# Kernel tuning notes

Measured on AMD Instinct MI355X. Metric: run time of the kernel, lower is better.

Reference implementation:

```python
import jax, jax.numpy as jnp
import numpy as np
from jax import lax

EPS = 1e-5


def _conv3x3(inp, w):
    # NCHW input, OIHW kernel, VALID padding, stride 1 (matches nn.Conv2d(k=3, s=1, p=0))
    return lax.conv_general_dilated(inp, w, (1, 1), 'VALID',
                                    dimension_numbers=('NCHW', 'OIHW', 'NCHW'))


def _bn(h, gamma, beta, mean, var):
    # inference-mode BatchNorm2d
    inv = gamma / jnp.sqrt(var + EPS)
    return h * inv[None, :, None, None] + (beta - mean * inv)[None, :, None, None]


def _xcorr_depthwise(zf, xf):
    # per-sample, per-channel sliding cross-correlation: template zf over search xf
    B, C, Hz, Wz = zf.shape
    _, _, Hx, Wx = xf.shape
    xr = xf.reshape(1, B * C, Hx, Wx)
    kr = zf.reshape(B * C, 1, Hz, Wz)
    out = lax.conv_general_dilated(xr, kr, (1, 1), 'VALID',
                                   feature_group_count=B * C,
                                   dimension_numbers=('NCHW', 'OIHW', 'NCHW'))
    return out.reshape(B, C, out.shape[2], out.shape[3])


def setup_inputs() -> dict:
    key = jax.random.key(0)
    ks = jax.random.split(key, 12)
    B, Cin, Ch = 64, 256, 256
    z = jax.random.normal(ks[0], (B, Cin, 16, 16), dtype=jnp.float32)
    x = jax.random.normal(ks[1], (B, Cin, 32, 32), dtype=jnp.float32)
    # conv weights ~ N(0, 0.01) as in _initialize_weights
    w_z = 0.01 * jax.random.normal(ks[2], (Ch, Cin, 3, 3), dtype=jnp.float32)
    w_x = 0.01 * jax.random.normal(ks[3], (Ch, Cin, 3, 3), dtype=jnp.float32)
    gamma_z = 0.5 + jax.random.uniform(ks[4], (Ch,), dtype=jnp.float32)
    beta_z = 0.1 * jax.random.normal(ks[5], (Ch,), dtype=jnp.float32)
    mean_z = 0.1 * jax.random.normal(ks[6], (Ch,), dtype=jnp.float32)
    var_z = 0.5 + jax.random.uniform(ks[7], (Ch,), dtype=jnp.float32)
    gamma_x = 0.5 + jax.random.uniform(ks[8], (Ch,), dtype=jnp.float32)
    beta_x = 0.1 * jax.random.normal(ks[9], (Ch,), dtype=jnp.float32)
    mean_x = 0.1 * jax.random.normal(ks[10], (Ch,), dtype=jnp.float32)
    var_x = 0.5 + jax.random.uniform(ks[11], (Ch,), dtype=jnp.float32)
    return {'z': z, 'x': x, 'w_z': w_z, 'w_x': w_x,
            'gamma_z': gamma_z, 'beta_z': beta_z, 'mean_z': mean_z, 'var_z': var_z,
            'gamma_x': gamma_x, 'beta_x': beta_x, 'mean_x': mean_x, 'var_x': var_x}


def reference(z, x, w_z, w_x, gamma_z, beta_z, mean_z, var_z,
              gamma_x, beta_x, mean_x, var_x):
    zf = _bn(_conv3x3(z, w_z), gamma_z, beta_z, mean_z, var_z)   # [B,C,14,14]
    xf = _bn(_conv3x3(x, w_x), gamma_x, beta_x, mean_x, var_x)   # [B,C,30,30]
    return _xcorr_depthwise(zf, xf)                               # [B,C,17,17]
```

## Files before the change

### kernel.cpp

```cpp
#include <hip/hip_runtime.h>
#include <cstdint>
#include <cstddef>

typedef _Float16 f16;
typedef _Float16 half4 __attribute__((ext_vector_type(4)));
typedef _Float16 half8 __attribute__((ext_vector_type(8)));
typedef float f32x4 __attribute__((ext_vector_type(4)));

#define BN_EPS 1e-5f

static constexpr size_t OFF_XB  = 0;
static constexpr size_t OFF_ZB  = 33554432;
static constexpr size_t OFF_WX  = 41943040;
static constexpr size_t OFF_WZ  = 43122688;
static constexpr size_t OFF_BNX = 44302336;
static constexpr size_t OFF_BNZ = 44304384;
static constexpr size_t OFF_XFH = 44306432;
static constexpr size_t OFF_ZFH = 75763712;

__global__ __launch_bounds__(256) void prep_all(
    const float* __restrict__ x, const float* __restrict__ z,
    const float* __restrict__ w_x, const float* __restrict__ w_z,
    const float* __restrict__ gx, const float* __restrict__ bx,
    const float* __restrict__ mx, const float* __restrict__ vx,
    const float* __restrict__ gz, const float* __restrict__ bz,
    const float* __restrict__ mz, const float* __restrict__ vz,
    f16* __restrict__ xb, f16* __restrict__ zb,
    f16* __restrict__ wxA, f16* __restrict__ wzA,
    float* __restrict__ bnx, float* __restrict__ bnz) {
  __shared__ float tile[64][33];
  const int bid = blockIdx.x;
  const int tid = threadIdx.x;
  if (bid < 12288) {
    const float* src; f16* dst; int lw, r;
    if (bid < 8192) { src = x; dst = xb; lw = 5; r = bid; }
    else            { src = z; dst = zb; lw = 4; r = bid - 8192; }
    const int W = 1 << lw;
    const int c0 = (r & 3) << 6;
    const int h = (r >> 2) & (W - 1);
    const int b = (r >> 2) >> lw;
    const float* sp = src + (size_t)(((b << 8) + c0) << lw << lw) + ((size_t)h << lw);
    const int n = W << 6;
    for (int i = tid; i < n; i += 256) {
      int cl = i >> lw, w = i & (W - 1);
      tile[cl][w] = sp[(size_t)cl << lw << lw | w];
    }
    __syncthreads();
    f16* dp = dst + ((size_t)((b << lw) + h) << lw << 8) + c0;
    for (int i = tid; i < n; i += 256) {
      int w = i >> 6, cl = i & 63;
      dp[(w << 8) + cl] = (f16)tile[cl][w];
    }
  } else if (bid < 16896) {
    int r = bid - 12288;
    const float* src = (r < 2304) ? w_x : w_z;
    f16* dst = (r < 2304) ? wxA : wzA;
    int rr = (r < 2304) ? r : r - 2304;
    int idx = rr * 256 + tid;
    int cin = idx & 255, cout = (idx >> 8) & 255, khw = idx >> 16;
    dst[idx] = (f16)src[(cout * 256 + cin) * 9 + khw];
  } else {
    int c = tid;
    float iv = gx[c] / sqrtf(vx[c] + BN_EPS);
    bnx[c] = iv;
    bnx[256 + c] = bx[c] - mx[c] * iv;
    float iz = gz[c] / sqrtf(vz[c] + BN_EPS);
    bnz[c] = iz;
    bnz[256 + c] = bz[c] - mz[c] * iz;
  }
}

__device__ __forceinline__ void gl_lds16(const f16* g, f16* l) {
  __builtin_amdgcn_global_load_lds((__attribute__((address_space(1))) void*)g,
                                   (__attribute__((address_space(3))) void*)l, 16, 0, 0);
}

__global__ __launch_bounds__(256, 4) void conv_gemm_u(
    const f16* __restrict__ xb, const f16* __restrict__ zb,
    const f16* __restrict__ wx, const f16* __restrict__ wz,
    const float* __restrict__ bnx, const float* __restrict__ bnz,
    f16* __restrict__ xfh, f16* __restrict__ zfh) {
  __shared__ f16 As[128 * 64];
  __shared__ f16 Bs[128 * 64];
  const int g = blockIdx.x;
  const int pairIdx = ((g >> 4) << 3) | (g & 7);
  const int mblk = (g >> 3) & 1;
  if (pairIdx >= 548) return;
  const f16* inp; const f16* wA; const float* bn; f16* out;
  int nblk, HIN, WIN, WOUT, NPIX, WPAD, OPLANE;
  if (pairIdx < 450) {
    inp = xb; wA = wx; bn = bnx; out = xfh; nblk = pairIdx;
    HIN = 32; WIN = 32; WOUT = 30; NPIX = 900; WPAD = 32; OPLANE = 960;
  } else {
    inp = zb; wA = wz; bn = bnz; out = zfh; nblk = pairIdx - 450;
    HIN = 16; WIN = 16; WOUT = 14; NPIX = 196; WPAD = 16; OPLANE = 224;
  }
  const int tid = threadIdx.x;
  const int wid = tid >> 6, lane = tid & 63;
  const int wm = (wid >> 1) << 6, wn = (wid & 1) << 6;
  const int q = lane >> 4, lm = lane & 15;
  const int sr = lane >> 3, sc = lane & 7;
  const int swz = (sc ^ sr) << 3;
  const int mbase = mblk << 7;

  int arow[4], brow[4];
#pragma unroll
  for (int l = 0; l < 4; ++l) {
    int rr = (wid << 5) + (l << 3) + sr;
    arow[l] = ((mbase + rr) << 8) + swz;
    int n = (nblk << 7) + rr;
    int b = n / NPIX, rem = n - b * NPIX;
    int oh = rem / WOUT, ow = rem - oh * WOUT;
    brow[l] = (((b * HIN + oh) * WIN + ow) << 8) + swz;
  }

  f32x4 acc[4][4] = {};
  const int cA0 = (q ^ (lm & 7)) << 3;

  for (int kt = 0; kt < 36; ++kt) {
    const int cinb = kt / 9;
    const int khw = kt - cinb * 9;
    const int cin0 = cinb << 6;
    const int kh = khw / 3, kw = khw - kh * 3;
    const int wofs = (khw << 16) + cin0;
    const int iofs = ((kh * WIN + kw) << 8) + cin0;
#pragma unroll
    for (int l = 0; l < 4; ++l) {
      const int ldso = ((wid << 5) + (l << 3)) << 6;
      gl_lds16(wA + wofs + arow[l], As + ldso);
      gl_lds16(inp + iofs + brow[l], Bs + ldso);
    }
    __syncthreads();
#pragma unroll
    for (int h = 0; h < 2; ++h) {
      const int co = cA0 ^ (h << 5);
      half8 af[4], bf[4];
#pragma unroll
      for (int f = 0; f < 4; ++f) {
        af[f] = *(const half8*)&As[((wm + (f << 4) + lm) << 6) + co];
        bf[f] = *(const half8*)&Bs[((wn + (f << 4) + lm) << 6) + co];
      }
#pragma unroll
      for (int fm = 0; fm < 4; ++fm)
#pragma unroll
        for (int fn = 0; fn < 4; ++fn)
          acc[fm][fn] =
              __builtin_amdgcn_mfma_f32_16x16x32_f16(af[fm], bf[fn], acc[fm][fn], 0, 0, 0);
    }
    __syncthreads();
  }

#pragma unroll
  for (int fn = 0; fn < 4; ++fn) {
    int n_g = (nblk << 7) + wn + (fn << 4) + lm;
    int b = n_g / NPIX, rem = n_g - b * NPIX;
    int oh = rem / WOUT, ow = rem - oh * WOUT;
    f16* op = out + (size_t)(b << 8) * OPLANE + oh * WPAD + ow;
#pragma unroll
    for (int fm = 0; fm < 4; ++fm) {
      int m0 = mbase + wm + (fm << 4) + (q << 2);
#pragma unroll
      for (int rg = 0; rg < 4; ++rg) {
        int m = m0 + rg;
        op[(size_t)m * OPLANE] = (f16)(acc[fm][fn][rg] * bn[m] + bn[256 + m]);
      }
    }
  }
}

static constexpr int XST = 40;
static constexpr int XCH = 30 * XST;
static constexpr int ZCH = 14 * 16;

__global__ __launch_bounds__(256) void xcorr_dw3(const f16* __restrict__ zfh,
                                                 const f16* __restrict__ xfh,
                                                 float* __restrict__ out) {
  __shared__ f16 xs[3 * XCH];
  __shared__ f16 zs[3 * ZCH];
  const int t = threadIdx.x;
  const int ch0 = blockIdx.x * 3;

  for (int i = t; i < 360; i += 256) {
    int ch = i / 120, rem = i - ch * 120;
    int row = rem >> 2, col = (rem & 3) << 3;
    if (ch0 + ch < 16384)
      *(half8*)(xs + ch * XCH + row * XST + col) =
          *(const half8*)(xfh + (size_t)(ch0 + ch) * 960 + row * 32 + col);
  }
  for (int i = t; i < 84; i += 256) {
    int ch = i / 28, rem = i - ch * 28;
    if (ch0 + ch < 16384)
      *(half8*)(zs + ch * ZCH + rem * 8) =
          *(const half8*)(zfh + (size_t)(ch0 + ch) * 224 + rem * 8);
  }
  __syncthreads();

  int lc = t / 85;
  int r = t - lc * 85;
  const bool ok = (lc < 3) && (ch0 + lc < 16384);
  if (lc > 2) lc = 2;
  const int oy = r / 5, oxq = r - oy * 5, ox0 = oxq * 4;
  const f16* xbp = xs + lc * XCH;
  const f16* zbp = zs + lc * ZCH;

  float acc[4] = {0.f, 0.f, 0.f, 0.f};

#pragma unroll 2
  for (int u = 0; u < 14; ++u) {
    float xr[20];
#pragma unroll
    for (int k = 0; k < 5; ++k) {
      half4 h = *(const half4*)(xbp + (oy + u) * XST + ox0 + k * 4);
#pragma unroll
      for (int e = 0; e < 4; ++e) xr[k * 4 + e] = (float)h[e];
    }
    float zc[14];
    {
      half8 z0 = *(const half8*)(zbp + u * 16);
      half8 z1 = *(const half8*)(zbp + u * 16 + 8);
#pragma unroll
      for (int e = 0; e < 8; ++e) zc[e] = (float)z0[e];
#pragma unroll
      for (int e = 0; e < 6; ++e) zc[8 + e] = (float)z1[e];
    }
#pragma unroll
    for (int v = 0; v < 14; ++v)
#pragma unroll
      for (int j = 0; j < 4; ++j) acc[j] = fmaf(zc[v], xr[v + j], acc[j]);
  }

  if (ok) {
    float* op = out + (size_t)(ch0 + lc) * 289 + oy * 17;
#pragma unroll
    for (int j = 0; j < 4; ++j) {
      int ox = ox0 + j;
      if (ox < 17) op[ox] = acc[j];
    }
  }
}

extern "C" void kernel_launch(void* const* d_in, const int* in_sizes, int n_in,
                              void* d_out, int out_size, void* d_ws, size_t ws_size,
                              hipStream_t stream) {
  const float* z = (const float*)d_in[0];
  const float* x = (const float*)d_in[1];
  const float* w_z = (const float*)d_in[2];
  const float* w_x = (const float*)d_in[3];
  const float* gamma_z = (const float*)d_in[4];
  const float* beta_z = (const float*)d_in[5];
  const float* mean_z = (const float*)d_in[6];
  const float* var_z = (const float*)d_in[7];
  const float* gamma_x = (const float*)d_in[8];
  const float* beta_x = (const float*)d_in[9];
  const float* mean_x = (const float*)d_in[10];
  const float* var_x = (const float*)d_in[11];

  char* ws = (char*)d_ws;
  f16* xb = (f16*)(ws + OFF_XB);
  f16* zb = (f16*)(ws + OFF_ZB);
  f16* wxA = (f16*)(ws + OFF_WX);
  f16* wzA = (f16*)(ws + OFF_WZ);
  float* bnx = (float*)(ws + OFF_BNX);
  float* bnz = (float*)(ws + OFF_BNZ);
  f16* xfh = (f16*)(ws + OFF_XFH);
  f16* zfh = (f16*)(ws + OFF_ZFH);
  float* out = (float*)d_out;

  prep_all<<<16897, 256, 0, stream>>>(x, z, w_x, w_z,
                                      gamma_x, beta_x, mean_x, var_x,
                                      gamma_z, beta_z, mean_z, var_z,
                                      xb, zb, wxA, wzA, bnx, bnz);

  conv_gemm_u<<<1104, 256, 0, stream>>>(xb, zb, wxA, wzA, bnx, bnz, xfh, zfh);

  xcorr_dw3<<<(16384 + 2) / 3, 256, 0, stream>>>(zfh, xfh, out);
}
```

Before: 310.9 us.

## Enlarge conv GEMM tile to full 256 output channels with double-buffered weights

After: 380.7 us. +22.5%, slower.

```diff
diff --git a/kernel.cpp b/kernel.cpp
--- a/kernel.cpp
+++ b/kernel.cpp
@@ -75,90 +75,104 @@
                                    (__attribute__((address_space(3))) void*)l, 16, 0, 0);
 }
 
-__global__ __launch_bounds__(256, 4) void conv_gemm_u(
+__global__ __launch_bounds__(256, 2) void conv_gemm_v3(
     const f16* __restrict__ xb, const f16* __restrict__ zb,
     const f16* __restrict__ wx, const f16* __restrict__ wz,
     const float* __restrict__ bnx, const float* __restrict__ bnz,
     f16* __restrict__ xfh, f16* __restrict__ zfh) {
-  __shared__ f16 As[128 * 64];
-  __shared__ f16 Bs[128 * 64];
-  const int g = blockIdx.x;
-  const int pairIdx = ((g >> 4) << 3) | (g & 7);
-  const int mblk = (g >> 3) & 1;
-  if (pairIdx >= 548) return;
+  __shared__ f16 As[2][256 * 64];
+  const int bid = blockIdx.x;
   const f16* inp; const f16* wA; const float* bn; f16* out;
   int nblk, HIN, WIN, WOUT, NPIX, WPAD, OPLANE;
-  if (pairIdx < 450) {
-    inp = xb; wA = wx; bn = bnx; out = xfh; nblk = pairIdx;
+  if (bid < 450) {
+    inp = xb; wA = wx; bn = bnx; out = xfh; nblk = bid;
     HIN = 32; WIN = 32; WOUT = 30; NPIX = 900; WPAD = 32; OPLANE = 960;
   } else {
-    inp = zb; wA = wz; bn = bnz; out = zfh; nblk = pairIdx - 450;
+    inp = zb; wA = wz; bn = bnz; out = zfh; nblk = bid - 450;
     HIN = 16; WIN = 16; WOUT = 14; NPIX = 196; WPAD = 16; OPLANE = 224;
   }
   const int tid = threadIdx.x;
   const int wid = tid >> 6, lane = tid & 63;
-  const int wm = (wid >> 1) << 6, wn = (wid & 1) << 6;
+  const int wml = (wid >> 1) << 7;
+  const int wnl = (wid & 1) << 6;
   const int q = lane >> 4, lm = lane & 15;
   const int sr = lane >> 3, sc = lane & 7;
   const int swz = (sc ^ sr) << 3;
-  const int mbase = mblk << 7;
-
-  int arow[4], brow[4];
-#pragma unroll
-  for (int l = 0; l < 4; ++l) {
-    int rr = (wid << 5) + (l << 3) + sr;
-    arow[l] = ((mbase + rr) << 8) + swz;
-    int n = (nblk << 7) + rr;
+
+  int arow[8];
+#pragma unroll
+  for (int l = 0; l < 8; ++l) {
+    int row = (wid << 6) + (l << 3) + sr;
+    arow[l] = (row << 8) + swz;
+  }
+  int ibase[4];
+#pragma unroll
+  for (int fn = 0; fn < 4; ++fn) {
+    int n = (nblk << 7) + wnl + (fn << 4) + lm;
     int b = n / NPIX, rem = n - b * NPIX;
     int oh = rem / WOUT, ow = rem - oh * WOUT;
-    brow[l] = (((b * HIN + oh) * WIN + ow) << 8) + swz;
-  }
-
-  f32x4 acc[4][4] = {};
-  const int cA0 = (q ^ (lm & 7)) << 3;
+    ibase[fn] = (((b * HIN + oh) * WIN + ow) << 8) + (q << 3);
+  }
+
+  f32x4 acc[8][4] = {};
+
+  {
+    const int wofs0 = 0 * 65536 + 0;
+#pragma unroll
+    for (int l = 0; l < 8; ++l)
+      gl_lds16(wA + wofs0 + arow[l], &As[0][((wid << 6) + (l << 3)) << 6]);
+  }
 
   for (int kt = 0; kt < 36; ++kt) {
+    const int p = kt & 1;
+    __syncthreads();
+
     const int cinb = kt / 9;
     const int khw = kt - cinb * 9;
-    const int cin0 = cinb << 6;
     const int kh = khw / 3, kw = khw - kh * 3;
-    const int wofs = (khw << 16) + cin0;
-    const int iofs = ((kh * WIN + kw) << 8) + cin0;
-#pragma unroll
-    for (int l = 0; l < 4; ++l) {
-      const int ldso = ((wid << 5) + (l << 3)) << 6;
-      gl_lds16(wA + wofs + arow[l], As + ldso);
-      gl_lds16(inp + iofs + brow[l], Bs + ldso);
-    }
-    __syncthreads();
+    const int iofs = ((kh * WIN + kw) << 8) + (cinb << 6);
+    half8 bf[4][2];
+#pragma unroll
+    for (int fn = 0; fn < 4; ++fn)
+#pragma unroll
+      for (int h = 0; h < 2; ++h)
+        bf[fn][h] = *(const half8*)(inp + ibase[fn] + iofs + (h << 5));
+
+    if (kt < 35) {
+      const int kt2 = kt + 1;
+      const int cinb2 = kt2 / 9;
+      const int khw2 = kt2 - cinb2 * 9;
+      const int wofs2 = (khw2 << 16) + (cinb2 << 6);
+#pragma unroll
+      for (int l = 0; l < 8; ++l)
+        gl_lds16(wA + wofs2 + arow[l], &As[p ^ 1][((wid << 6) + (l << 3)) << 6]);
+    }
+
 #pragma unroll
     for (int h = 0; h < 2; ++h) {
-      const int co = cA0 ^ (h << 5);
-      half8 af[4], bf[4];
-#pragma unroll
-      for (int f = 0; f < 4; ++f) {
-        af[f] = *(const half8*)&As[((wm + (f << 4) + lm) << 6) + co];
-        bf[f] = *(const half8*)&Bs[((wn + (f << 4) + lm) << 6) + co];
-      }
-#pragma unroll
-      for (int fm = 0; fm < 4; ++fm)
+      const int co = ((((h << 2) + q) ^ (lm & 7)) << 3);
+      half8 af[8];
+#pragma unroll
+      for (int fm = 0; fm < 8; ++fm)
+        af[fm] = *(const half8*)&As[p][((wml + (fm << 4) + lm) << 6) + co];
+#pragma unroll
+      for (int fm = 0; fm < 8; ++fm)
 #pragma unroll
         for (int fn = 0; fn < 4; ++fn)
-          acc[fm][fn] =
-              __builtin_amdgcn_mfma_f32_16x16x32_f16(af[fm], bf[fn], acc[fm][fn], 0, 0, 0);
-    }
-    __syncthreads();
+          acc[fm][fn] = __builtin_amdgcn_mfma_f32_16x16x32_f16(af[fm], bf[fn][h],
+                                                               acc[fm][fn], 0, 0, 0);
+    }
   }
 
 #pragma unroll
   for (int fn = 0; fn < 4; ++fn) {
-    int n_g = (nblk << 7) + wn + (fn << 4) + lm;
+    int n_g = (nblk << 7) + wnl + (fn << 4) + lm;
     int b = n_g / NPIX, rem = n_g - b * NPIX;
     int oh = rem / WOUT, ow = rem - oh * WOUT;
     f16* op = out + (size_t)(b << 8) * OPLANE + oh * WPAD + ow;
 #pragma unroll
-    for (int fm = 0; fm < 4; ++fm) {
-      int m0 = mbase + wm + (fm << 4) + (q << 2);
+    for (int fm = 0; fm < 8; ++fm) {
+      int m0 = wml + (fm << 4) + (q << 2);
 #pragma unroll
       for (int rg = 0; rg < 4; ++rg) {
         int m = m0 + rg;
@@ -271,7 +285,7 @@
                                       gamma_z, beta_z, mean_z, var_z,
                                       xb, zb, wxA, wzA, bnx, bnz);
 
-  conv_gemm_u<<<1104, 256, 0, stream>>>(xb, zb, wxA, wzA, bnx, bnz, xfh, zfh);
+  conv_gemm_v3<<<548, 256, 0, stream>>>(xb, zb, wxA, wzA, bnx, bnz, xfh, zfh);
 
   xcorr_dw3<<<(16384 + 2) / 3, 256, 0, stream>>>(zfh, xfh, out);
 }
```
